# Kernel optimization log

Measured on AMD Instinct MI355X. Metric: run time of the kernel, lower is better.

The kernel has to match this reference:

```python
import jax, jax.numpy as jnp
import numpy as np

B, T, F, U = 32768, 7, 36, 256

def setup_inputs() -> dict:
    key = jax.random.key(0)
    ks = jax.random.split(key, 5)
    x = jax.random.normal(ks[0], (B, T, F), dtype=jnp.float32)
    h0 = jax.random.normal(ks[1], (B, U), dtype=jnp.float32)
    c0 = jax.random.normal(ks[2], (B, U), dtype=jnp.float32)
    Wk = jax.random.normal(ks[3], (F, 4 * U), dtype=jnp.float32) * 0.1
    Wr = jax.random.normal(ks[4], (U, 4 * U), dtype=jnp.float32) * 0.05
    b = jnp.zeros((4 * U,), dtype=jnp.float32)
    return {"x": x, "h0": h0, "c0": c0, "Wk": Wk, "Wr": Wr, "b": b}

def reference(x, h0, c0, Wk, Wr, b):
    # Precompute input projection for all 7 steps: [B,T,4U]
    zx = jnp.einsum('btf,fg->btg', x, Wk) + b
    zx_t = jnp.transpose(zx, (1, 0, 2))  # time-major [T,B,4U]

    def step(carry, z_in):
        h, c = carry
        z = z_in + h @ Wr  # [B,4U]
        i, f, g, o = jnp.split(z, 4, axis=-1)  # Keras gate order i,f,g,o
        i = jax.nn.sigmoid(i)
        f = jax.nn.sigmoid(f)
        g = jnp.tanh(g)
        o = jax.nn.sigmoid(o)
        c_new = f * c + i * g
        h_new = o * jnp.tanh(c_new)
        return (h_new, c_new), h_new

    (_, _), hs = jax.lax.scan(step, (h0, c0), zx_t)
    return jnp.transpose(hs, (1, 0, 2))  # [B,T,U] (return_sequences=True)
```

## Files before the change

kernel.cpp:

```cpp
#include <hip/hip_runtime.h>
#include <hip/hip_bf16.h>

typedef _Float16 half8 __attribute__((ext_vector_type(8)));
typedef float f32x4 __attribute__((ext_vector_type(4)));

#define B_TOTAL 32768
#define T 7
#define F 36
#define U 256
#define G4 1024
#define BM 64
#define KC 10
#define KPACK 32
#define H_STRIDE 264
#define X_STRIDE 72

__global__ __launch_bounds__(1024) void pack_w(const float* __restrict__ Wr,
                                               const float* __restrict__ Wk,
                                               _Float16* __restrict__ Wq) {
    const int kc   = blockIdx.x >> 2;
    const int kin0 = (blockIdx.x & 3) * 8;
    const int n    = threadIdx.x;
    _Float16* dst = Wq + ((size_t)kc * G4 + n) * KPACK + kin0;
    #pragma unroll
    for (int j = 0; j < 8; ++j) {
        int k = kc * KPACK + kin0 + j;
        float v = 0.f;
        if (k < U)          v = Wr[(size_t)k * G4 + n];
        else if (k < U + F) v = Wk[(size_t)(k - U) * G4 + n];
        dst[j] = (_Float16)v;
    }
}

__device__ __forceinline__ float fast_sigmoid(float x) {
    return __builtin_amdgcn_rcpf(1.f + __expf(-x));
}
__device__ __forceinline__ float fast_tanh(float x) {
    return 1.f - 2.f * __builtin_amdgcn_rcpf(1.f + __expf(2.f * x));
}

__global__ __launch_bounds__(1024) void lstm_kernel(
    const float* __restrict__ x,
    const float* __restrict__ h0,
    const float* __restrict__ c0,
    const _Float16* __restrict__ Wq,
    const float* __restrict__ bias_g,
    float* __restrict__ out)
{
    __shared__ __align__(16) _Float16 hA[BM * H_STRIDE];
    __shared__ __align__(16) _Float16 xA[BM * X_STRIDE];

    const int tid  = threadIdx.x;
    const int lane = tid & 63;
    const int w    = tid >> 6;
    const int l15  = lane & 15;
    const int q    = lane >> 4;
    const int u0   = w * 16;
    const int b0   = blockIdx.x * BM;

    for (int i = tid; i < BM * U; i += 1024) {
        int m = i >> 8, u = i & 255;
        hA[m * H_STRIDE + u] = (_Float16)h0[(size_t)b0 * U + i];
    }
    for (int i = tid; i < BM * (64 - F); i += 1024) {
        int m = i / (64 - F), f = i % (64 - F);
        xA[m * X_STRIDE + F + f] = (_Float16)0.f;
    }
    for (int i = tid; i < BM * F; i += 1024) {
        int m = i / F, f = i % F;
        xA[m * X_STRIDE + f] = (_Float16)x[((size_t)(b0 + m) * T) * F + f];
    }
    float c[16];
    #pragma unroll
    for (int mt = 0; mt < 4; ++mt)
        #pragma unroll
        for (int r = 0; r < 4; ++r) {
            int row = mt * 16 + q * 4 + r;
            c[mt * 4 + r] = c0[(size_t)(b0 + row) * U + u0 + l15];
        }
    float bv[4];
    #pragma unroll
    for (int g = 0; g < 4; ++g) bv[g] = bias_g[g * U + u0 + l15];

    __syncthreads();

    for (int t = 0; t < T; ++t) {
        f32x4 acc[4][4];
        #pragma unroll
        for (int mt = 0; mt < 4; ++mt)
            #pragma unroll
            for (int g = 0; g < 4; ++g)
                acc[mt][g] = (f32x4){bv[g], bv[g], bv[g], bv[g]};

        float xp0 = 0.f, xp1 = 0.f, xp2 = 0.f;
        if (t + 1 < T) {
            {
                int i = tid;        int m = i / F, f = i % F;
                xp0 = x[((size_t)(b0 + m) * T + t + 1) * F + f];
            }
            {
                int i = tid + 1024; int m = i / F, f = i % F;
                xp1 = x[((size_t)(b0 + m) * T + t + 1) * F + f];
            }
            if (tid < BM * F - 2048) {
                int i = tid + 2048; int m = i / F, f = i % F;
                xp2 = x[((size_t)(b0 + m) * T + t + 1) * F + f];
            }
        }

        #pragma unroll 2
        for (int kc = 0; kc < KC; ++kc) {
            half8 bf[4];
            #pragma unroll
            for (int g = 0; g < 4; ++g) {
                size_t off = ((size_t)kc * G4 + g * U + u0 + l15) * KPACK + q * 8;
                bf[g] = *(const half8*)(Wq + off);
            }
            #pragma unroll
            for (int mt = 0; mt < 4; ++mt) {
                half8 af;
                if (kc < 8)
                    af = *(const half8*)&hA[(mt * 16 + l15) * H_STRIDE + kc * 32 + q * 8];
                else
                    af = *(const half8*)&xA[(mt * 16 + l15) * X_STRIDE + (kc - 8) * 32 + q * 8];
                #pragma unroll
                for (int g = 0; g < 4; ++g)
                    acc[mt][g] = __builtin_amdgcn_mfma_f32_16x16x32_f16(af, bf[g], acc[mt][g], 0, 0, 0);
            }
        }

        float hnew[16];
        #pragma unroll
        for (int mt = 0; mt < 4; ++mt)
            #pragma unroll
            for (int r = 0; r < 4; ++r) {
                float zi = acc[mt][0][r];
                float zf = acc[mt][1][r];
                float zg = acc[mt][2][r];
                float zo = acc[mt][3][r];
                float ig = fast_sigmoid(zi);
                float fg = fast_sigmoid(zf);
                float gg = fast_tanh(zg);
                float og = fast_sigmoid(zo);
                float cn = fg * c[mt * 4 + r] + ig * gg;
                c[mt * 4 + r] = cn;
                hnew[mt * 4 + r] = og * fast_tanh(cn);
            }

        __syncthreads();

        #pragma unroll
        for (int mt = 0; mt < 4; ++mt)
            #pragma unroll
            for (int r = 0; r < 4; ++r) {
                int row = mt * 16 + q * 4 + r;
                hA[row * H_STRIDE + u0 + l15] = (_Float16)hnew[mt * 4 + r];
            }
        if (t + 1 < T) {
            { int i = tid;        int m = i / F, f = i % F; xA[m * X_STRIDE + f] = (_Float16)xp0; }
            { int i = tid + 1024; int m = i / F, f = i % F; xA[m * X_STRIDE + f] = (_Float16)xp1; }
            if (tid < BM * F - 2048) {
                int i = tid + 2048; int m = i / F, f = i % F;
                xA[m * X_STRIDE + f] = (_Float16)xp2;
            }
        }
        __syncthreads();

        #pragma unroll
        for (int rb = 0; rb < 2; ++rb) {
            int j   = tid + rb * 1024;
            int row = j >> 5;
            int uo  = (j & 31) * 8;
            half8 hv = *(const half8*)&hA[row * H_STRIDE + uo];
            f32x4 lo = { (float)hv[0], (float)hv[1], (float)hv[2], (float)hv[3] };
            f32x4 hi = { (float)hv[4], (float)hv[5], (float)hv[6], (float)hv[7] };
            float* dst = out + ((size_t)(b0 + row) * T + t) * U + uo;
            *(f32x4*)dst       = lo;
            *(f32x4*)(dst + 4) = hi;
        }
    }
}

extern "C" void kernel_launch(void* const* d_in, const int* in_sizes, int n_in,
                              void* d_out, int out_size, void* d_ws, size_t ws_size,
                              hipStream_t stream) {
    const float* x  = (const float*)d_in[0];
    const float* h0 = (const float*)d_in[1];
    const float* c0 = (const float*)d_in[2];
    const float* Wk = (const float*)d_in[3];
    const float* Wr = (const float*)d_in[4];
    const float* b  = (const float*)d_in[5];
    float* out = (float*)d_out;

    _Float16* Wq = (_Float16*)d_ws;

    pack_w<<<KC * 4, 1024, 0, stream>>>(Wr, Wk, Wq);
    lstm_kernel<<<B_TOTAL / BM, 1024, 0, stream>>>(x, h0, c0, Wq, b, out);
}
```

Baseline: 514.6 us.

## Restructure LSTM kernel: 32-row tiles, double-buffered h, direct x loads and output writes

Shrinks each block to 32 batch rows and 512 threads, with each wave covering 32 hidden units across two row tiles. The packed weights are rearranged per wave so B-fragment loads are contiguous. h is double-buffered in shared memory so only one barrier is needed per timestep. x is read straight from global memory into registers instead of being staged in shared memory, and h is written to the output directly from the gate computation in fp32 instead of through a shared-memory readback. The goal is fewer barriers, more blocks per CU and less LDS traffic. In exchange, the output stores are scattered 4-byte writes and twice as many blocks each re-read the weights.

```diff
diff --git a/kernel.cpp b/kernel.cpp
--- a/kernel.cpp
+++ b/kernel.cpp
@@ -1,5 +1,4 @@
 #include <hip/hip_runtime.h>
-#include <hip/hip_bf16.h>
 
 typedef _Float16 half8 __attribute__((ext_vector_type(8)));
 typedef float f32x4 __attribute__((ext_vector_type(4)));
@@ -9,27 +8,29 @@
 #define F 36
 #define U 256
 #define G4 1024
-#define BM 64
+#define BM 32
+#define THREADS 512
 #define KC 10
-#define KPACK 32
 #define H_STRIDE 264
-#define X_STRIDE 72
 
-__global__ __launch_bounds__(1024) void pack_w(const float* __restrict__ Wr,
-                                               const float* __restrict__ Wk,
-                                               _Float16* __restrict__ Wq) {
-    const int kc   = blockIdx.x >> 2;
-    const int kin0 = (blockIdx.x & 3) * 8;
-    const int n    = threadIdx.x;
-    _Float16* dst = Wq + ((size_t)kc * G4 + n) * KPACK + kin0;
-    #pragma unroll
-    for (int j = 0; j < 8; ++j) {
-        int k = kc * KPACK + kin0 + j;
-        float v = 0.f;
-        if (k < U)          v = Wr[(size_t)k * G4 + n];
-        else if (k < U + F) v = Wk[(size_t)(k - U) * G4 + n];
-        dst[j] = (_Float16)v;
-    }
+__global__ __launch_bounds__(512) void pack_w(const float* __restrict__ Wr,
+                                              const float* __restrict__ Wk,
+                                              _Float16* __restrict__ Wq) {
+    const int bid = blockIdx.x;
+    const int gnt = bid & 7;
+    const int kc  = (bid >> 3) % KC;
+    const int w   = (bid >> 3) / KC;
+    const int tid = threadIdx.x;
+    const int l15 = tid >> 5;
+    const int kin = tid & 31;
+    const int g  = gnt >> 1;
+    const int nt = gnt & 1;
+    const int col = g * 256 + w * 32 + nt * 16 + l15;
+    const int k   = kc * 32 + kin;
+    float v = 0.f;
+    if (k < U)          v = Wr[(size_t)k * G4 + col];
+    else if (k < U + F) v = Wk[(size_t)(k - U) * G4 + col];
+    Wq[(size_t)bid * 512 + tid] = (_Float16)v;
 }
 
 __device__ __forceinline__ float fast_sigmoid(float x) {
@@ -39,7 +40,7 @@
     return 1.f - 2.f * __builtin_amdgcn_rcpf(1.f + __expf(2.f * x));
 }
 
-__global__ __launch_bounds__(1024) void lstm_kernel(
+__global__ __launch_bounds__(512, 4) void lstm_kernel(
     const float* __restrict__ x,
     const float* __restrict__ h0,
     const float* __restrict__ c0,
@@ -47,137 +48,134 @@
     const float* __restrict__ bias_g,
     float* __restrict__ out)
 {
-    __shared__ __align__(16) _Float16 hA[BM * H_STRIDE];
-    __shared__ __align__(16) _Float16 xA[BM * X_STRIDE];
+    __shared__ __align__(16) _Float16 hbuf[2][BM * H_STRIDE];
 
     const int tid  = threadIdx.x;
     const int lane = tid & 63;
     const int w    = tid >> 6;
     const int l15  = lane & 15;
     const int q    = lane >> 4;
-    const int u0   = w * 16;
+    const int u0   = w * 32;
     const int b0   = blockIdx.x * BM;
 
-    for (int i = tid; i < BM * U; i += 1024) {
+    for (int i = tid; i < BM * U; i += THREADS) {
         int m = i >> 8, u = i & 255;
-        hA[m * H_STRIDE + u] = (_Float16)h0[(size_t)b0 * U + i];
+        hbuf[0][m * H_STRIDE + u] = (_Float16)h0[(size_t)b0 * U + i];
     }
-    for (int i = tid; i < BM * (64 - F); i += 1024) {
-        int m = i / (64 - F), f = i % (64 - F);
-        xA[m * X_STRIDE + F + f] = (_Float16)0.f;
-    }
-    for (int i = tid; i < BM * F; i += 1024) {
-        int m = i / F, f = i % F;
-        xA[m * X_STRIDE + f] = (_Float16)x[((size_t)(b0 + m) * T) * F + f];
-    }
-    float c[16];
+    float c[2][2][4];
     #pragma unroll
-    for (int mt = 0; mt < 4; ++mt)
+    for (int mt = 0; mt < 2; ++mt)
         #pragma unroll
-        for (int r = 0; r < 4; ++r) {
-            int row = mt * 16 + q * 4 + r;
-            c[mt * 4 + r] = c0[(size_t)(b0 + row) * U + u0 + l15];
-        }
-    float bv[4];
+        for (int nt = 0; nt < 2; ++nt)
+            #pragma unroll
+            for (int r = 0; r < 4; ++r) {
+                int row = mt * 16 + q * 4 + r;
+                c[mt][nt][r] = c0[(size_t)(b0 + row) * U + u0 + nt * 16 + l15];
+            }
+    float bv[4][2];
     #pragma unroll
-    for (int g = 0; g < 4; ++g) bv[g] = bias_g[g * U + u0 + l15];
+    for (int g = 0; g < 4; ++g)
+        #pragma unroll
+        for (int nt = 0; nt < 2; ++nt)
+            bv[g][nt] = bias_g[g * 256 + u0 + nt * 16 + l15];
+
+    const _Float16* wbase = Wq + (size_t)w * (KC * 8 * 512) + (l15 * 32 + q * 8);
 
     __syncthreads();
 
+    int cur = 0;
+    #pragma unroll 1
     for (int t = 0; t < T; ++t) {
-        f32x4 acc[4][4];
+        f32x4 acc[2][8];
         #pragma unroll
-        for (int mt = 0; mt < 4; ++mt)
+        for (int mt = 0; mt < 2; ++mt)
             #pragma unroll
-            for (int g = 0; g < 4; ++g)
-                acc[mt][g] = (f32x4){bv[g], bv[g], bv[g], bv[g]};
+            for (int gnt = 0; gnt < 8; ++gnt) {
+                float v = bv[gnt >> 1][gnt & 1];
+                acc[mt][gnt] = (f32x4){v, v, v, v};
+            }
 
-        float xp0 = 0.f, xp1 = 0.f, xp2 = 0.f;
-        if (t + 1 < T) {
-            {
-                int i = tid;        int m = i / F, f = i % F;
-                xp0 = x[((size_t)(b0 + m) * T + t + 1) * F + f];
+        #pragma unroll
+        for (int kc = 0; kc < 8; ++kc) {
+            half8 a0 = *(const half8*)&hbuf[cur][(l15)      * H_STRIDE + kc * 32 + q * 8];
+            half8 a1 = *(const half8*)&hbuf[cur][(16 + l15) * H_STRIDE + kc * 32 + q * 8];
+            half8 bfr[4];
+            #pragma unroll
+            for (int gnt = 0; gnt < 4; ++gnt)
+                bfr[gnt] = *(const half8*)(wbase + (size_t)(kc * 8 + gnt) * 512);
+            #pragma unroll
+            for (int gnt = 0; gnt < 4; ++gnt) {
+                acc[0][gnt] = __builtin_amdgcn_mfma_f32_16x16x32_f16(a0, bfr[gnt], acc[0][gnt], 0, 0, 0);
+                acc[1][gnt] = __builtin_amdgcn_mfma_f32_16x16x32_f16(a1, bfr[gnt], acc[1][gnt], 0, 0, 0);
             }
-            {
-                int i = tid + 1024; int m = i / F, f = i % F;
-                xp1 = x[((size_t)(b0 + m) * T + t + 1) * F + f];
-            }
-            if (tid < BM * F - 2048) {
-                int i = tid + 2048; int m = i / F, f = i % F;
-                xp2 = x[((size_t)(b0 + m) * T + t + 1) * F + f];
+            #pragma unroll
+            for (int gnt = 0; gnt < 4; ++gnt)
+                bfr[gnt] = *(const half8*)(wbase + (size_t)(kc * 8 + 4 + gnt) * 512);
+            #pragma unroll
+            for (int gnt = 0; gnt < 4; ++gnt) {
+                acc[0][4 + gnt] = __builtin_amdgcn_mfma_f32_16x16x32_f16(a0, bfr[gnt], acc[0][4 + gnt], 0, 0, 0);
+                acc[1][4 + gnt] = __builtin_amdgcn_mfma_f32_16x16x32_f16(a1, bfr[gnt], acc[1][4 + gnt], 0, 0, 0);
             }
         }
 
-        #pragma unroll 2
-        for (int kc = 0; kc < KC; ++kc) {
-            half8 bf[4];
+        half8 xf[2], xg[2];
+        #pragma unroll
+        for (int mt = 0; mt < 2; ++mt) {
+            const float* xr = x + ((size_t)(b0 + mt * 16 + l15) * T + t) * F;
+            f32x4 v0 = *(const f32x4*)(xr + q * 8);
+            f32x4 v1 = *(const f32x4*)(xr + q * 8 + 4);
+            half8 hv;
             #pragma unroll
-            for (int g = 0; g < 4; ++g) {
-                size_t off = ((size_t)kc * G4 + g * U + u0 + l15) * KPACK + q * 8;
-                bf[g] = *(const half8*)(Wq + off);
+            for (int j = 0; j < 4; ++j) { hv[j] = (_Float16)v0[j]; hv[4 + j] = (_Float16)v1[j]; }
+            xf[mt] = hv;
+            half8 hz;
+            #pragma unroll
+            for (int j = 0; j < 8; ++j) hz[j] = (_Float16)0.f;
+            if (q == 0) {
+                f32x4 v2 = *(const f32x4*)(xr + 32);
+                #pragma unroll
+                for (int j = 0; j < 4; ++j) hz[j] = (_Float16)v2[j];
             }
-            #pragma unroll
-            for (int mt = 0; mt < 4; ++mt) {
-                half8 af;
-                if (kc < 8)
-                    af = *(const half8*)&hA[(mt * 16 + l15) * H_STRIDE + kc * 32 + q * 8];
-                else
-                    af = *(const half8*)&xA[(mt * 16 + l15) * X_STRIDE + (kc - 8) * 32 + q * 8];
-                #pragma unroll
-                for (int g = 0; g < 4; ++g)
-                    acc[mt][g] = __builtin_amdgcn_mfma_f32_16x16x32_f16(af, bf[g], acc[mt][g], 0, 0, 0);
-            }
+            xg[mt] = hz;
+        }
+        #pragma unroll
+        for (int gnt = 0; gnt < 8; ++gnt) {
+            half8 b8 = *(const half8*)(wbase + (size_t)(8 * 8 + gnt) * 512);
+            acc[0][gnt] = __builtin_amdgcn_mfma_f32_16x16x32_f16(xf[0], b8, acc[0][gnt], 0, 0, 0);
+            acc[1][gnt] = __builtin_amdgcn_mfma_f32_16x16x32_f16(xf[1], b8, acc[1][gnt], 0, 0, 0);
+        }
+        #pragma unroll
+        for (int gnt = 0; gnt < 8; ++gnt) {
+            half8 b9 = *(const half8*)(wbase + (size_t)(9 * 8 + gnt) * 512);
+            acc[0][gnt] = __builtin_amdgcn_mfma_f32_16x16x32_f16(xg[0], b9, acc[0][gnt], 0, 0, 0);
+            acc[1][gnt] = __builtin_amdgcn_mfma_f32_16x16x32_f16(xg[1], b9, acc[1][gnt], 0, 0, 0);
         }
 
-        float hnew[16];
+        const int nxt = cur ^ 1;
         #pragma unroll
-        for (int mt = 0; mt < 4; ++mt)
+        for (int mt = 0; mt < 2; ++mt)
             #pragma unroll
-            for (int r = 0; r < 4; ++r) {
-                float zi = acc[mt][0][r];
-                float zf = acc[mt][1][r];
-                float zg = acc[mt][2][r];
-                float zo = acc[mt][3][r];
-                float ig = fast_sigmoid(zi);
-                float fg = fast_sigmoid(zf);
-                float gg = fast_tanh(zg);
-                float og = fast_sigmoid(zo);
-                float cn = fg * c[mt * 4 + r] + ig * gg;
-                c[mt * 4 + r] = cn;
-                hnew[mt * 4 + r] = og * fast_tanh(cn);
-            }
+            for (int nt = 0; nt < 2; ++nt)
+                #pragma unroll
+                for (int r = 0; r < 4; ++r) {
+                    float zi = acc[mt][0 + nt][r];
+                    float zf = acc[mt][2 + nt][r];
+                    float zg = acc[mt][4 + nt][r];
+                    float zo = acc[mt][6 + nt][r];
+                    float ig = fast_sigmoid(zi);
+                    float fg = fast_sigmoid(zf);
+                    float gg = fast_tanh(zg);
+                    float og = fast_sigmoid(zo);
+                    float cn = fg * c[mt][nt][r] + ig * gg;
+                    c[mt][nt][r] = cn;
+                    float hv = og * fast_tanh(cn);
+                    int row = mt * 16 + q * 4 + r;
+                    hbuf[nxt][row * H_STRIDE + u0 + nt * 16 + l15] = (_Float16)hv;
+                    out[((size_t)(b0 + row) * T + t) * U + u0 + nt * 16 + l15] = hv;
+                }
 
         __syncthreads();
-
-        #pragma unroll
-        for (int mt = 0; mt < 4; ++mt)
-            #pragma unroll
-            for (int r = 0; r < 4; ++r) {
-                int row = mt * 16 + q * 4 + r;
-                hA[row * H_STRIDE + u0 + l15] = (_Float16)hnew[mt * 4 + r];
-            }
-        if (t + 1 < T) {
-            { int i = tid;        int m = i / F, f = i % F; xA[m * X_STRIDE + f] = (_Float16)xp0; }
-            { int i = tid + 1024; int m = i / F, f = i % F; xA[m * X_STRIDE + f] = (_Float16)xp1; }
-            if (tid < BM * F - 2048) {
-                int i = tid + 2048; int m = i / F, f = i % F;
-                xA[m * X_STRIDE + f] = (_Float16)xp2;
-            }
-        }
-        __syncthreads();
-
-        #pragma unroll
-        for (int rb = 0; rb < 2; ++rb) {
-            int j   = tid + rb * 1024;
-            int row = j >> 5;
-            int uo  = (j & 31) * 8;
-            half8 hv = *(const half8*)&hA[row * H_STRIDE + uo];
-            f32x4 lo = { (float)hv[0], (float)hv[1], (float)hv[2], (float)hv[3] };
-            f32x4 hi = { (float)hv[4], (float)hv[5], (float)hv[6], (float)hv[7] };
-            float* dst = out + ((size_t)(b0 + row) * T + t) * U + uo;
-            *(f32x4*)dst       = lo;
-            *(f32x4*)(dst + 4) = hi;
-        }
+        cur = nxt;
     }
 }
 
@@ -194,6 +192,6 @@
 
     _Float16* Wq = (_Float16*)d_ws;
 
-    pack_w<<<KC * 4, 1024, 0, stream>>>(Wr, Wk, Wq);
-    lstm_kernel<<<B_TOTAL / BM, 1024, 0, stream>>>(x, h0, c0, Wq, b, out);
+    pack_w<<<8 * KC * 8, 512, 0, stream>>>(Wr, Wk, Wq);
+    lstm_kernel<<<B_TOTAL / BM, 512, 0, stream>>>(x, h0, c0, Wq, b, out);
 }
```

Measured after the change: 1.747 ms. +239.5%, slower.
